# Kernel tuning notes

Measured on AMD Instinct MI355X. Metric: run time of the kernel, lower is better.

The kernel has to match this reference:

```python
import jax, jax.numpy as jnp
import numpy as np

HEAD = 8

def setup_inputs() -> dict:
    key = jax.random.key(0)
    ks = jax.random.split(key, 11)
    B, C, W, H = 16, 512, 32, 32
    d, N = C // HEAD, W * H
    return {
        "x": jax.random.normal(ks[0], (B, C, W, H), jnp.float32),
        "Wq": jax.random.normal(ks[1], (C, C), jnp.float32) * 0.02,
        "bq": jax.random.normal(ks[2], (C,), jnp.float32) * 0.02,
        "Wk": jax.random.normal(ks[3], (C, C), jnp.float32) * 0.02,
        "bk": jax.random.normal(ks[4], (C,), jnp.float32) * 0.02,
        "Wv": jax.random.normal(ks[5], (C, C), jnp.float32) * 0.02,
        "bv": jax.random.normal(ks[6], (C,), jnp.float32) * 0.02,
        "rel_h": jax.random.normal(ks[7], (1, HEAD, d, 1, H), jnp.float32),
        "rel_w": jax.random.normal(ks[8], (1, HEAD, d, W, 1), jnp.float32),
        "reg_qk": jax.random.normal(ks[9], (1, N, N), jnp.float32),
        "reg_v": jax.random.normal(ks[10], (1, d, N), jnp.float32),
    }

def reference(x, Wq, bq, Wk, bk, Wv, bv, rel_h, rel_w, reg_qk, reg_v):
    B, C, W, H = x.shape
    head = HEAD
    d = C // head
    N = W * H
    def conv1x1(inp, Wt, b):  # 1x1 conv == per-pixel linear
        return jnp.einsum('bchw,oc->bohw', inp, Wt) + b[None, :, None, None]
    q = conv1x1(x, Wq, bq).reshape(B, head, d, N)
    k = conv1x1(x, Wk, bk).reshape(B, head, d, N)
    v = conv1x1(x, Wv, bv).reshape(B, head, d, N)
    # content-content: q^T k -> [B, head, N, N]
    cc = jnp.einsum('bhdn,bhdm->bhnm', q, k)
    # content-position: (rel_h + rel_w) broadcast to [1, head, d, W, H] -> [head, N, d]
    pos = (rel_h + rel_w).reshape(head, d, N)
    cp = jnp.einsum('hdn,bhdm->bhnm', pos, q)
    energy = cc + cp  # [B, head, N, N]
    n_reg = reg_qk.shape[0]
    energy = jnp.concatenate(
        [energy, jnp.broadcast_to(reg_qk[None], (B, n_reg, N, N))], axis=1)
    v_all = jnp.concatenate(
        [v, jnp.broadcast_to(reg_v[None], (B, n_reg, d, N))], axis=1)
    attn = jax.nn.softmax(energy, axis=-1)  # [B, head+n_reg, N, N]
    # v @ attn^T
    out = jnp.einsum('bgdn,bgmn->bgdm', v_all, attn)
    out = out[:, :head].reshape(B, C, W, H)
    return out + x
```

## Files before the change

### kernel.cpp

```cpp
#include <hip/hip_runtime.h>

#define BB   16
#define HEADS 8
#define DH   64
#define NSP  1024
#define CCH  512

typedef unsigned int   u32;
typedef unsigned short u16;
typedef __attribute__((ext_vector_type(8))) short  short8;
typedef __attribute__((ext_vector_type(4))) float  floatx4;
typedef __attribute__((ext_vector_type(2))) unsigned uint2v;

#if defined(__has_builtin)
#if __has_builtin(__builtin_amdgcn_exp2f)
#define EXP2F(x) __builtin_amdgcn_exp2f(x)
#else
#define EXP2F(x) exp2f(x)
#endif
#if __has_builtin(__builtin_amdgcn_permlane32_swap)
#define HAVE_PL32 1
#endif
#if __has_builtin(__builtin_amdgcn_permlane16_swap)
#define HAVE_PL16 1
#endif
#else
#define EXP2F(x) exp2f(x)
#endif

__device__ __forceinline__ u16 f2b(float f) {
  u32 x = __float_as_uint(f);
  x = x + 0x7fffu + ((x >> 16) & 1u);
  return (u16)(x >> 16);
}

__device__ __forceinline__ u32 pkbf(float lo, float hi) {
  return __builtin_amdgcn_perm(__float_as_uint(hi) + 0x8000u,
                               __float_as_uint(lo) + 0x8000u, 0x07060302u);
}

__device__ __forceinline__ void gload_lds16(const u16* g, u16* l) {
  __builtin_amdgcn_global_load_lds((const __attribute__((address_space(1))) u32*)g,
                                   (__attribute__((address_space(3))) u32*)l, 16, 0, 0);
}

__device__ __forceinline__ void lane32_swap(u32 a, u32 b, u32& ap, u32& bp, bool hi32) {
#ifdef HAVE_PL32
  uint2v r = __builtin_amdgcn_permlane32_swap(a, b, false, false);
  ap = r.x; bp = r.y;
  (void)hi32;
#else
  u32 sb = (u32)__shfl_xor((int)b, 32);
  u32 sa = (u32)__shfl_xor((int)a, 32);
  ap = hi32 ? sb : a;
  bp = hi32 ? b : sa;
#endif
}

__device__ __forceinline__ u32 lane16_xor(u32 x, bool qodd) {
#ifdef HAVE_PL16
  uint2v r = __builtin_amdgcn_permlane16_swap(x, x, false, false);
  return qodd ? r.x : r.y;
#else
  return (u32)__shfl_xor((int)x, 16);
#endif
}

__global__ __launch_bounds__(256) void prep_all(const float* __restrict__ x,
                                                const float* __restrict__ Wq,
                                                const float* __restrict__ Wk,
                                                const float* __restrict__ Wv,
                                                const float* __restrict__ rel_h,
                                                const float* __restrict__ rel_w,
                                                u16* __restrict__ wbf,
                                                u16* __restrict__ pos,
                                                u16* __restrict__ xt) {
  __shared__ float ld[64][68];
  int bid = blockIdx.x;
  int t = threadIdx.x;
  if (bid < 768) {
    int idx = bid * 256 + t;
    int which = idx >> 16;
    int r4 = (idx & 65535) * 4;
    const float* src = which == 0 ? Wq : which == 1 ? Wk : Wv;
    float4 v = *(const float4*)&src[r4];
    ushort4 s;
    s.x = f2b(v.x); s.y = f2b(v.y); s.z = f2b(v.z); s.w = f2b(v.w);
    *(ushort4*)&wbf[(which << 18) + r4] = s;
  } else if (bid < 2816) {
    int idx = (bid - 768) * 256 + t;
    int dd = idx & 63;
    int n  = (idx >> 6) & 1023;
    int h  = idx >> 16;
    int ww = n >> 5, hh = n & 31;
    float v = rel_h[(h * 64 + dd) * 32 + hh] + rel_w[(h * 64 + dd) * 32 + ww];
    pos[idx] = f2b(v);
  } else {
    int bid2 = bid - 2816;
    int ntile = bid2 & 15, ctile = (bid2 >> 4) & 7, b = bid2 >> 7;
    const float* xb = x + (((size_t)b * CCH + ctile * 64) << 10) + ntile * 64;
#pragma unroll
    for (int p = 0; p < 4; ++p) {
      int c = p * 16 + (t >> 4), n4 = (t & 15) * 4;
      float4 v = *(const float4*)&xb[((size_t)c << 10) + n4];
      ld[c][n4 + 0] = v.x; ld[c][n4 + 1] = v.y; ld[c][n4 + 2] = v.z; ld[c][n4 + 3] = v.w;
    }
    __syncthreads();
    u16* xo = xt + (((size_t)b << 10) + ntile * 64) * CCH + ctile * 64;
#pragma unroll
    for (int p = 0; p < 2; ++p) {
      int id = p * 256 + t;
      int n = id >> 3, c8 = (id & 7) * 8;
      ushort4 s0, s1;
      s0.x = f2b(ld[c8 + 0][n]); s0.y = f2b(ld[c8 + 1][n]);
      s0.z = f2b(ld[c8 + 2][n]); s0.w = f2b(ld[c8 + 3][n]);
      s1.x = f2b(ld[c8 + 4][n]); s1.y = f2b(ld[c8 + 5][n]);
      s1.z = f2b(ld[c8 + 6][n]); s1.w = f2b(ld[c8 + 7][n]);
      *(ushort4*)&xo[(size_t)n * CCH + c8] = s0;
      *(ushort4*)&xo[(size_t)n * CCH + c8 + 4] = s1;
    }
  }
}

__global__ __launch_bounds__(256, 2) void qkv_fused(const u16* __restrict__ wbf,
                                                    const u16* __restrict__ xt,
                                                    const float* __restrict__ bq,
                                                    const float* __restrict__ bk,
                                                    const float* __restrict__ bv,
                                                    u16* __restrict__ qw,
                                                    u16* __restrict__ kw,
                                                    u16* __restrict__ vtw) {
  int hid = blockIdx.x;
  int xcd  = hid & 7;
  int slot = hid >> 3;
  int otile = slot & 7;
  int pair  = xcd * 16 + (slot >> 3);
  int ntile = pair & 7;
  int b     = pair >> 3;
  int o0 = otile * 64, n0 = ntile * 128;

  __shared__ __align__(16) u16 smem[2 * 20480];

  int t = threadIdx.x;
  int w = t >> 6, lane = t & 63;
  int l15 = lane & 15, quad = lane >> 4;
  int srow = lane >> 3, sc = lane & 7;
  int scc = (sc ^ srow) << 3;

  floatx4 aq[8], ak[8], av[8];
#pragma unroll
  for (int i = 0; i < 8; ++i) {
    aq[i] = (floatx4){0.f, 0.f, 0.f, 0.f};
    ak[i] = (floatx4){0.f, 0.f, 0.f, 0.f};
    av[i] = (floatx4){0.f, 0.f, 0.f, 0.f};
  }

  auto stage = [&](int k0, int buf) {
    u16* base = smem + buf * 20480;
#pragma unroll
    for (int p = 0; p < 10; ++p) {
      int g0 = w * 80 + p * 8;
      if (g0 < 192) {
        int which = g0 >> 6;
        int r0 = g0 & 63;
        gload_lds16(wbf + ((size_t)which << 18) + (size_t)(o0 + r0 + srow) * CCH + k0 + scc,
                    base + which * 4096 + r0 * 64);
      } else {
        int r0 = g0 - 192;
        gload_lds16(xt + (size_t)(b * 1024 + n0 + r0 + srow) * CCH + k0 + scc,
                    base + 12288 + r0 * 64);
      }
    }
  };

  int rs = l15 & 7;
  int c0 = (quad ^ rs) << 3;
  int c1 = ((4 + quad) ^ rs) << 3;
  int wrow = (w * 16 + l15) * 64;

  stage(0, 0);
  stage(64, 1);

  for (int ki = 0; ki < 8; ++ki) {
    if (ki < 7) asm volatile("s_waitcnt vmcnt(10)" ::: "memory");
    else        asm volatile("s_waitcnt vmcnt(0)" ::: "memory");
    __builtin_amdgcn_s_barrier();
    __builtin_amdgcn_sched_barrier(0);

    u16* base = smem + (ki & 1) * 20480;
    u16* Xb = base + 12288;
    __builtin_amdgcn_s_setprio(1);
#pragma unroll
    for (int ks = 0; ks < 2; ++ks) {
      int cc = ks ? c1 : c0;
      short8 fq = *(short8*)&base[wrow + cc];
      short8 fk = *(short8*)&base[4096 + wrow + cc];
      short8 fv = *(short8*)&base[8192 + wrow + cc];
#pragma unroll
      for (int ns = 0; ns < 8; ++ns) {
        short8 fx = *(short8*)&Xb[(ns * 16 + l15) * 64 + cc];
        aq[ns] = __builtin_amdgcn_mfma_f32_16x16x32_bf16(fq, fx, aq[ns], 0, 0, 0);
        ak[ns] = __builtin_amdgcn_mfma_f32_16x16x32_bf16(fk, fx, ak[ns], 0, 0, 0);
        av[ns] = __builtin_amdgcn_mfma_f32_16x16x32_bf16(fx, fv, av[ns], 0, 0, 0);
      }
    }
    __builtin_amdgcn_s_setprio(0);

    if (ki < 6) {
      __builtin_amdgcn_sched_barrier(0);
      __builtin_amdgcn_s_barrier();
      stage((ki + 2) * 64, ki & 1);
    }
  }

  __syncthreads();
  u16* epQ = smem;
  u16* epK = smem + 9216;
  u16* epV = smem + 18432;
  {
    int ob = o0 + w * 16 + quad * 4;
    float q0 = bq[ob], q1 = bq[ob + 1], q2 = bq[ob + 2], q3 = bq[ob + 3];
    float k0b = bk[ob], k1b = bk[ob + 1], k2b = bk[ob + 2], k3b = bk[ob + 3];
    float vb = bv[o0 + w * 16 + l15];
#pragma unroll
    for (int ns = 0; ns < 8; ++ns) {
      int n = ns * 16 + l15;
      uint2 pk;
      pk.x = pkbf(aq[ns][0] + q0, aq[ns][1] + q1);
      pk.y = pkbf(aq[ns][2] + q2, aq[ns][3] + q3);
      *(uint2*)&epQ[n * 72 + w * 16 + quad * 4] = pk;
      pk.x = pkbf(ak[ns][0] + k0b, ak[ns][1] + k1b);
      pk.y = pkbf(ak[ns][2] + k2b, ak[ns][3] + k3b);
      *(uint2*)&epK[n * 72 + w * 16 + quad * 4] = pk;
      pk.x = pkbf(av[ns][0] + vb, av[ns][1] + vb);
      pk.y = pkbf(av[ns][2] + vb, av[ns][3] + vb);
      *(uint2*)&epV[(w * 16 + l15) * 136 + ns * 16 + quad * 4] = pk;
    }
  }
  __syncthreads();
  int h = otile;
  {
    int row = t >> 1, half = t & 1;
    size_t gb = ((size_t)(b * HEADS + h) * NSP + n0 + row) * 64 + half * 32;
#pragma unroll
    for (int i = 0; i < 4; ++i)
      *(uint4*)&qw[gb + i * 8] = *(uint4*)&epQ[row * 72 + half * 32 + i * 8];
#pragma unroll
    for (int i = 0; i < 4; ++i)
      *(uint4*)&kw[gb + i * 8] = *(uint4*)&epK[row * 72 + half * 32 + i * 8];
  }
  {
    int row = t >> 2, q4 = t & 3;
#pragma unroll
    for (int i = 0; i < 4; ++i) {
      int nl = q4 * 32 + i * 8;
      int n = n0 + nl;
      int ntl = n >> 6, nn = n & 63;
      *(uint4*)&vtw[(((size_t)(b * HEADS + h) * 16 + ntl) * 64 + row) * 64 + nn]
          = *(uint4*)&epV[row * 136 + nl];
    }
  }
}

__global__ __launch_bounds__(256, 2) void attn_mfma(const u16* __restrict__ qw,
                                                    const u16* __restrict__ kw,
                                                    const u16* __restrict__ vtw,
                                                    const u16* __restrict__ pos,
                                                    const float* __restrict__ x,
                                                    float* __restrict__ out) {
  int bh = blockIdx.x, mtile = blockIdx.y;
  int b = bh >> 3, h = bh & 7;
  __shared__ __align__(16) u16 smem_u16[36864];

  int t = threadIdx.x;
  int w = t >> 6, lane = t & 63;
  int l15 = lane & 15, quad = lane >> 4;
  bool qodd = (quad & 1) != 0;
  bool hi32 = lane >= 32;
  size_t bhs = (size_t)bh;

  short8 qa[4][2], pa[4][2];
  {
    const short* qg = (const short*)qw + (bhs * NSP + mtile * 256 + w * 64) * 64;
    const short* pg = (const short*)pos + ((size_t)h * NSP + mtile * 256 + w * 64) * 64;
#pragma unroll
    for (int msub = 0; msub < 4; ++msub)
#pragma unroll
      for (int ks = 0; ks < 2; ++ks) {
        int off = (msub * 16 + l15) * 64 + ks * 32 + quad * 8;
        qa[msub][ks] = *(const short8*)(qg + off);
        pa[msub][ks] = *(const short8*)(pg + off);
      }
  }

  floatx4 oacc[4][4];
  float lsum[4] = {0.f, 0.f, 0.f, 0.f};
#pragma unroll
  for (int i = 0; i < 4; ++i)
#pragma unroll
    for (int j = 0; j < 4; ++j) oacc[i][j] = (floatx4){0.f, 0.f, 0.f, 0.f};

  const u16* kg  = kw + bhs * NSP * 64;
  const u16* qgn = qw + bhs * NSP * 64;
  const u16* vg  = vtw + bhs * 16 * 4096;
  int srow = lane >> 3, sc = lane & 7;

  int rs = l15 & 7;
  int c0 = (quad ^ rs) << 3;
  int c1 = ((4 + quad) ^ rs) << 3;

  auto stage = [&](int nt, int buf) {
    u16* kt = smem_u16 + buf * 12288;
    u16* qt = kt + 4096;
    u16* vt = qt + 4096;
#pragma unroll
    for (int p = 0; p < 2; ++p) {
      int r0 = w * 16 + p * 8;
      int row = r0 + srow;
      int swz = ((sc ^ (row & 7)) << 3);
      gload_lds16(kg + (nt * 64 + row) * 64 + swz, &kt[r0 * 64]);
      gload_lds16(qgn + (nt * 64 + row) * 64 + swz, &qt[r0 * 64]);
      gload_lds16(vg + (size_t)nt * 4096 + row * 64 + swz, &vt[r0 * 64]);
    }
  };

  stage(0, 0);
  stage(1, 1);

  for (int nt = 0; nt < 16; ++nt) {
    __builtin_amdgcn_s_barrier();
    if (nt < 14) {
      stage(nt + 2, (nt + 2) % 3);
      asm volatile("s_waitcnt vmcnt(12)" ::: "memory");
    } else if (nt == 14) {
      asm volatile("s_waitcnt vmcnt(6)" ::: "memory");
    } else {
      asm volatile("s_waitcnt vmcnt(0)" ::: "memory");
    }
    __builtin_amdgcn_sched_barrier(0);

    u16* kt = smem_u16 + (nt % 3) * 12288;
    u16* qt = kt + 4096;
    u16* vt = qt + 4096;

#pragma unroll
    for (int half = 0; half < 2; ++half) {
      u32 Wd[4][4];
#pragma unroll
      for (int nblk2 = 0; nblk2 < 2; ++nblk2) {
        int nblk = half * 2 + nblk2;
        int rb = (nblk * 16 + l15) * 64;
        short8 kb0 = *(short8*)&kt[rb + c0];
        short8 kb1 = *(short8*)&kt[rb + c1];
        short8 qb0 = *(short8*)&qt[rb + c0];
        short8 qb1 = *(short8*)&qt[rb + c1];
        floatx4 sc4[4];
        __builtin_amdgcn_s_setprio(1);
#pragma unroll
        for (int msub = 0; msub < 4; ++msub) {
          floatx4 c = (floatx4){0.f, 0.f, 0.f, 0.f};
          c = __builtin_amdgcn_mfma_f32_16x16x32_bf16(kb0, qa[msub][0], c, 0, 0, 0);
          c = __builtin_amdgcn_mfma_f32_16x16x32_bf16(kb1, qa[msub][1], c, 0, 0, 0);
          c = __builtin_amdgcn_mfma_f32_16x16x32_bf16(qb0, pa[msub][0], c, 0, 0, 0);
          c = __builtin_amdgcn_mfma_f32_16x16x32_bf16(qb1, pa[msub][1], c, 0, 0, 0);
          sc4[msub] = c;
        }
        __builtin_amdgcn_s_setprio(0);
#pragma unroll
        for (int msub = 0; msub < 4; ++msub) {
          float p0 = EXP2F(fmaf(sc4[msub][0], 1.44269504f, -11.5415603f));
          float p1 = EXP2F(fmaf(sc4[msub][1], 1.44269504f, -11.5415603f));
          float p2 = EXP2F(fmaf(sc4[msub][2], 1.44269504f, -11.5415603f));
          float p3 = EXP2F(fmaf(sc4[msub][3], 1.44269504f, -11.5415603f));
          lsum[msub] += (p0 + p1) + (p2 + p3);
          Wd[msub][nblk2 * 2 + 0] = pkbf(p0, p1);
          Wd[msub][nblk2 * 2 + 1] = pkbf(p2, p3);
        }
      }
      short8 pB[4];
#pragma unroll
      for (int msub = 0; msub < 4; ++msub) {
        u32 A0p, B0p, A1p, B1p;
        lane32_swap(Wd[msub][0], Wd[msub][2], A0p, B0p, hi32);
        lane32_swap(Wd[msub][1], Wd[msub][3], A1p, B1p, hi32);
        u32 G0 = lane16_xor(qodd ? A0p : B0p, qodd);
        u32 G1 = lane16_xor(qodd ? A1p : B1p, qodd);
        union { u32 u[4]; short8 s; } cvt;
        cvt.u[0] = qodd ? G0 : A0p;
        cvt.u[1] = qodd ? G1 : A1p;
        cvt.u[2] = qodd ? B0p : G0;
        cvt.u[3] = qodd ? B1p : G1;
        pB[msub] = cvt.s;
      }
      __builtin_amdgcn_s_setprio(1);
#pragma unroll
      for (int dd = 0; dd < 4; ++dd) {
        int row = dd * 16 + l15;
        short8 vb = *(short8*)&vt[row * 64 + (((half * 4 + quad) ^ (row & 7)) << 3)];
#pragma unroll
        for (int msub = 0; msub < 4; ++msub)
          oacc[msub][dd] = __builtin_amdgcn_mfma_f32_16x16x32_bf16(vb, pB[msub], oacc[msub][dd], 0, 0, 0);
      }
      __builtin_amdgcn_s_setprio(0);
    }
  }

  float rinv[4];
#pragma unroll
  for (int msub = 0; msub < 4; ++msub) {
    float l = lsum[msub];
    l += __shfl_xor(l, 16);
    l += __shfl_xor(l, 32);
    rinv[msub] = 1.0f / l;
  }

  __syncthreads();
  float* ot = (float*)smem_u16 + w * 2304;
  int l8 = lane & 7, lr = lane >> 3;
#pragma unroll
  for (int mh = 0; mh < 2; ++mh) {
#pragma unroll
    for (int ms2 = 0; ms2 < 2; ++ms2) {
      int msub = mh * 2 + ms2;
#pragma unroll
      for (int dd = 0; dd < 4; ++dd)
#pragma unroll
        for (int r = 0; r < 4; ++r)
          ot[(dd * 16 + quad * 4 + r) * 36 + ms2 * 16 + l15] = oacc[msub][dd][r] * rinv[msub];
    }
#pragma unroll
    for (int pass = 0; pass < 8; ++pass) {
      int dd = pass * 8 + lr;
      float4 o4 = *(float4*)&ot[dd * 36 + l8 * 4];
      size_t off = (((size_t)b * CCH + h * DH + dd) << 10) + mtile * 256 + w * 64 + mh * 32 + l8 * 4;
      float4 xv = *(const float4*)&x[off];
      o4.x += xv.x; o4.y += xv.y; o4.z += xv.z; o4.w += xv.w;
      *(float4*)&out[off] = o4;
    }
  }
}

extern "C" void kernel_launch(void* const* d_in, const int* in_sizes, int n_in,
                              void* d_out, int out_size, void* d_ws, size_t ws_size,
                              hipStream_t stream) {
  const float* x     = (const float*)d_in[0];
  const float* Wq    = (const float*)d_in[1];
  const float* bq    = (const float*)d_in[2];
  const float* Wk    = (const float*)d_in[3];
  const float* bk    = (const float*)d_in[4];
  const float* Wv    = (const float*)d_in[5];
  const float* bv    = (const float*)d_in[6];
  const float* rel_h = (const float*)d_in[7];
  const float* rel_w = (const float*)d_in[8];
  float* out = (float*)d_out;

  char* ws = (char*)d_ws;
  u16* qw   = (u16*)(ws);
  u16* kw   = (u16*)(ws + ((size_t)16 << 20));
  u16* vtw  = (u16*)(ws + ((size_t)32 << 20));
  u16* pos  = (u16*)(ws + ((size_t)48 << 20));
  u16* wbf  = (u16*)(ws + ((size_t)49 << 20));
  u16* xt   = (u16*)d_out;

  hipLaunchKernelGGL(prep_all, dim3(4864), dim3(256), 0, stream,
                     x, Wq, Wk, Wv, rel_h, rel_w, wbf, pos, xt);
  hipLaunchKernelGGL(qkv_fused, dim3(1024), dim3(256), 0, stream,
                     wbf, xt, bq, bk, bv, qw, kw, vtw);
  hipLaunchKernelGGL(attn_mfma, dim3(128, 4), dim3(256), 0, stream,
                     qw, kw, vtw, pos, x, out);
}
```

Baseline: 208.0 us.

## Switch attention kernel to 32x32x16 MFMA tiles and drop setprio hints

```diff
diff --git a/kernel.cpp b/kernel.cpp
--- a/kernel.cpp
+++ b/kernel.cpp
@@ -10,6 +10,7 @@
 typedef unsigned short u16;
 typedef __attribute__((ext_vector_type(8))) short  short8;
 typedef __attribute__((ext_vector_type(4))) float  floatx4;
+typedef __attribute__((ext_vector_type(16))) float floatx16;
 typedef __attribute__((ext_vector_type(2))) unsigned uint2v;
 
 #if defined(__has_builtin)
@@ -20,9 +21,6 @@
 #endif
 #if __has_builtin(__builtin_amdgcn_permlane32_swap)
 #define HAVE_PL32 1
-#endif
-#if __has_builtin(__builtin_amdgcn_permlane16_swap)
-#define HAVE_PL16 1
 #endif
 #else
 #define EXP2F(x) exp2f(x)
@@ -54,15 +52,6 @@
   u32 sa = (u32)__shfl_xor((int)a, 32);
   ap = hi32 ? sb : a;
   bp = hi32 ? b : sa;
-#endif
-}
-
-__device__ __forceinline__ u32 lane16_xor(u32 x, bool qodd) {
-#ifdef HAVE_PL16
-  uint2v r = __builtin_amdgcn_permlane16_swap(x, x, false, false);
-  return qodd ? r.x : r.y;
-#else
-  return (u32)__shfl_xor((int)x, 16);
 #endif
 }
 
@@ -189,7 +178,6 @@
 
     u16* base = smem + (ki & 1) * 20480;
     u16* Xb = base + 12288;
-    __builtin_amdgcn_s_setprio(1);
 #pragma unroll
     for (int ks = 0; ks < 2; ++ks) {
       int cc = ks ? c1 : c0;
@@ -204,7 +192,6 @@
         av[ns] = __builtin_amdgcn_mfma_f32_16x16x32_bf16(fx, fv, av[ns], 0, 0, 0);
       }
     }
-    __builtin_amdgcn_s_setprio(0);
 
     if (ki < 6) {
       __builtin_amdgcn_sched_barrier(0);
@@ -274,40 +261,38 @@
 
   int t = threadIdx.x;
   int w = t >> 6, lane = t & 63;
-  int l15 = lane & 15, quad = lane >> 4;
-  bool qodd = (quad & 1) != 0;
-  bool hi32 = lane >= 32;
+  int l31 = lane & 31, hi1 = lane >> 5;
+  int hi8 = hi1 * 8;
+  bool hi32 = hi1 != 0;
   size_t bhs = (size_t)bh;
 
-  short8 qa[4][2], pa[4][2];
+  short8 qa[2][4], pa[2][4];
   {
     const short* qg = (const short*)qw + (bhs * NSP + mtile * 256 + w * 64) * 64;
     const short* pg = (const short*)pos + ((size_t)h * NSP + mtile * 256 + w * 64) * 64;
 #pragma unroll
-    for (int msub = 0; msub < 4; ++msub)
-#pragma unroll
-      for (int ks = 0; ks < 2; ++ks) {
-        int off = (msub * 16 + l15) * 64 + ks * 32 + quad * 8;
+    for (int msub = 0; msub < 2; ++msub)
+#pragma unroll
+      for (int ks = 0; ks < 4; ++ks) {
+        int off = (msub * 32 + l31) * 64 + ks * 16 + hi8;
         qa[msub][ks] = *(const short8*)(qg + off);
         pa[msub][ks] = *(const short8*)(pg + off);
       }
   }
 
-  floatx4 oacc[4][4];
-  float lsum[4] = {0.f, 0.f, 0.f, 0.f};
-#pragma unroll
-  for (int i = 0; i < 4; ++i)
-#pragma unroll
-    for (int j = 0; j < 4; ++j) oacc[i][j] = (floatx4){0.f, 0.f, 0.f, 0.f};
+  floatx16 oacc[2][2];
+  float lsum[2] = {0.f, 0.f};
+#pragma unroll
+  for (int i = 0; i < 2; ++i)
+#pragma unroll
+    for (int j = 0; j < 2; ++j)
+#pragma unroll
+      for (int r = 0; r < 16; ++r) oacc[i][j][r] = 0.f;
 
   const u16* kg  = kw + bhs * NSP * 64;
   const u16* qgn = qw + bhs * NSP * 64;
   const u16* vg  = vtw + bhs * 16 * 4096;
   int srow = lane >> 3, sc = lane & 7;
-
-  int rs = l15 & 7;
-  int c0 = (quad ^ rs) << 3;
-  int c1 = ((4 + quad) ^ rs) << 3;
 
   auto stage = [&](int nt, int buf) {
     u16* kt = smem_u16 + buf * 12288;
@@ -344,72 +329,66 @@
     u16* vt = qt + 4096;
 
 #pragma unroll
-    for (int half = 0; half < 2; ++half) {
-      u32 Wd[4][4];
-#pragma unroll
-      for (int nblk2 = 0; nblk2 < 2; ++nblk2) {
-        int nblk = half * 2 + nblk2;
-        int rb = (nblk * 16 + l15) * 64;
-        short8 kb0 = *(short8*)&kt[rb + c0];
-        short8 kb1 = *(short8*)&kt[rb + c1];
-        short8 qb0 = *(short8*)&qt[rb + c0];
-        short8 qb1 = *(short8*)&qt[rb + c1];
-        floatx4 sc4[4];
-        __builtin_amdgcn_s_setprio(1);
-#pragma unroll
-        for (int msub = 0; msub < 4; ++msub) {
-          floatx4 c = (floatx4){0.f, 0.f, 0.f, 0.f};
-          c = __builtin_amdgcn_mfma_f32_16x16x32_bf16(kb0, qa[msub][0], c, 0, 0, 0);
-          c = __builtin_amdgcn_mfma_f32_16x16x32_bf16(kb1, qa[msub][1], c, 0, 0, 0);
-          c = __builtin_amdgcn_mfma_f32_16x16x32_bf16(qb0, pa[msub][0], c, 0, 0, 0);
-          c = __builtin_amdgcn_mfma_f32_16x16x32_bf16(qb1, pa[msub][1], c, 0, 0, 0);
-          sc4[msub] = c;
+    for (int nsub = 0; nsub < 2; ++nsub) {
+      short8 kf[4], qf[4];
+      int rowA = nsub * 32 + l31, rx7 = rowA & 7;
+#pragma unroll
+      for (int ks = 0; ks < 4; ++ks) {
+        int ad = rowA * 64 + (((ks * 2 + hi1) ^ rx7) << 3);
+        kf[ks] = *(short8*)&kt[ad];
+        qf[ks] = *(short8*)&qt[ad];
+      }
+      short8 pv0[2], pv1[2];
+#pragma unroll
+      for (int msub = 0; msub < 2; ++msub) {
+        floatx16 c;
+#pragma unroll
+        for (int r = 0; r < 16; ++r) c[r] = 0.f;
+#pragma unroll
+        for (int ks = 0; ks < 4; ++ks)
+          c = __builtin_amdgcn_mfma_f32_32x32x16_bf16(kf[ks], qa[msub][ks], c, 0, 0, 0);
+#pragma unroll
+        for (int ks = 0; ks < 4; ++ks)
+          c = __builtin_amdgcn_mfma_f32_32x32x16_bf16(qf[ks], pa[msub][ks], c, 0, 0, 0);
+        float p[16];
+#pragma unroll
+        for (int r = 0; r < 16; ++r)
+          p[r] = EXP2F(fmaf(c[r], 1.44269504f, -11.5415603f));
+        lsum[msub] += (((p[0] + p[1]) + (p[2] + p[3])) + ((p[4] + p[5]) + (p[6] + p[7])))
+                    + (((p[8] + p[9]) + (p[10] + p[11])) + ((p[12] + p[13]) + (p[14] + p[15])));
+        u32 wp[8];
+#pragma unroll
+        for (int i = 0; i < 8; ++i) wp[i] = pkbf(p[2 * i], p[2 * i + 1]);
+        u32 x0, y0, x1, y1, x2, y2, x3, y3;
+        lane32_swap(wp[0], wp[2], x0, y0, hi32);
+        lane32_swap(wp[1], wp[3], x1, y1, hi32);
+        lane32_swap(wp[4], wp[6], x2, y2, hi32);
+        lane32_swap(wp[5], wp[7], x3, y3, hi32);
+        union { u32 u[4]; short8 s; } cv0, cv1;
+        cv0.u[0] = x0; cv0.u[1] = x1; cv0.u[2] = y0; cv0.u[3] = y1;
+        cv1.u[0] = x2; cv1.u[1] = x3; cv1.u[2] = y2; cv1.u[3] = y3;
+        pv0[msub] = cv0.s;
+        pv1[msub] = cv1.s;
+      }
+#pragma unroll
+      for (int ddsub = 0; ddsub < 2; ++ddsub) {
+        int rowV = ddsub * 32 + l31, rv7 = rowV & 7;
+        int ksb = nsub * 2;
+        short8 v0 = *(short8*)&vt[rowV * 64 + ((((ksb + 0) * 2 + hi1) ^ rv7) << 3)];
+        short8 v1 = *(short8*)&vt[rowV * 64 + ((((ksb + 1) * 2 + hi1) ^ rv7) << 3)];
+#pragma unroll
+        for (int msub = 0; msub < 2; ++msub) {
+          oacc[msub][ddsub] = __builtin_amdgcn_mfma_f32_32x32x16_bf16(v0, pv0[msub], oacc[msub][ddsub], 0, 0, 0);
+          oacc[msub][ddsub] = __builtin_amdgcn_mfma_f32_32x32x16_bf16(v1, pv1[msub], oacc[msub][ddsub], 0, 0, 0);
         }
-        __builtin_amdgcn_s_setprio(0);
-#pragma unroll
-        for (int msub = 0; msub < 4; ++msub) {
-          float p0 = EXP2F(fmaf(sc4[msub][0], 1.44269504f, -11.5415603f));
-          float p1 = EXP2F(fmaf(sc4[msub][1], 1.44269504f, -11.5415603f));
-          float p2 = EXP2F(fmaf(sc4[msub][2], 1.44269504f, -11.5415603f));
-          float p3 = EXP2F(fmaf(sc4[msub][3], 1.44269504f, -11.5415603f));
-          lsum[msub] += (p0 + p1) + (p2 + p3);
-          Wd[msub][nblk2 * 2 + 0] = pkbf(p0, p1);
-          Wd[msub][nblk2 * 2 + 1] = pkbf(p2, p3);
-        }
-      }
-      short8 pB[4];
-#pragma unroll
-      for (int msub = 0; msub < 4; ++msub) {
-        u32 A0p, B0p, A1p, B1p;
-        lane32_swap(Wd[msub][0], Wd[msub][2], A0p, B0p, hi32);
-        lane32_swap(Wd[msub][1], Wd[msub][3], A1p, B1p, hi32);
-        u32 G0 = lane16_xor(qodd ? A0p : B0p, qodd);
-        u32 G1 = lane16_xor(qodd ? A1p : B1p, qodd);
-        union { u32 u[4]; short8 s; } cvt;
-        cvt.u[0] = qodd ? G0 : A0p;
-        cvt.u[1] = qodd ? G1 : A1p;
-        cvt.u[2] = qodd ? B0p : G0;
-        cvt.u[3] = qodd ? B1p : G1;
-        pB[msub] = cvt.s;
-      }
-      __builtin_amdgcn_s_setprio(1);
-#pragma unroll
-      for (int dd = 0; dd < 4; ++dd) {
-        int row = dd * 16 + l15;
-        short8 vb = *(short8*)&vt[row * 64 + (((half * 4 + quad) ^ (row & 7)) << 3)];
-#pragma unroll
-        for (int msub = 0; msub < 4; ++msub)
-          oacc[msub][dd] = __builtin_amdgcn_mfma_f32_16x16x32_bf16(vb, pB[msub], oacc[msub][dd], 0, 0, 0);
-      }
-      __builtin_amdgcn_s_setprio(0);
-    }
-  }
-
-  float rinv[4];
-#pragma unroll
-  for (int msub = 0; msub < 4; ++msub) {
+      }
+    }
+  }
+
+  float rinv[2];
+#pragma unroll
+  for (int msub = 0; msub < 2; ++msub) {
     float l = lsum[msub];
-    l += __shfl_xor(l, 16);
     l += __shfl_xor(l, 32);
     rinv[msub] = 1.0f / l;
   }
@@ -420,14 +399,12 @@
 #pragma unroll
   for (int mh = 0; mh < 2; ++mh) {
 #pragma unroll
-    for (int ms2 = 0; ms2 < 2; ++ms2) {
-      int msub = mh * 2 + ms2;
-#pragma unroll
-      for (int dd = 0; dd < 4; ++dd)
-#pragma unroll
-        for (int r = 0; r < 4; ++r)
-          ot[(dd * 16 + quad * 4 + r) * 36 + ms2 * 16 + l15] = oacc[msub][dd][r] * rinv[msub];
-    }
+    for (int ddsub = 0; ddsub < 2; ++ddsub)
+#pragma unroll
+      for (int r = 0; r < 16; ++r) {
+        int dd = ddsub * 32 + (r & 3) + 8 * (r >> 2) + 4 * hi1;
+        ot[dd * 36 + l31] = oacc[mh][ddsub][r] * rinv[mh];
+      }
 #pragma unroll
     for (int pass = 0; pass < 8; ++pass) {
       int dd = pass * 8 + lr;
```

Result: slower. 216.8 us (+4.2%).

## Pre-swizzle Q/K/V/pos into MFMA fragment layout and load directly to registers

Applied to the files above, without the earlier changes.

```diff
diff --git a/kernel.cpp b/kernel.cpp
--- a/kernel.cpp
+++ b/kernel.cpp
@@ -65,6 +65,7 @@
   return (u32)__shfl_xor((int)x, 16);
 #endif
 }
+
 
 __global__ __launch_bounds__(256) void prep_all(const float* __restrict__ x,
                                                 const float* __restrict__ Wq,
@@ -91,10 +92,13 @@
     int idx = (bid - 768) * 256 + t;
     int dd = idx & 63;
     int n  = (idx >> 6) & 1023;
-    int h  = idx >> 16;
+    int hd = idx >> 16;
     int ww = n >> 5, hh = n & 31;
-    float v = rel_h[(h * 64 + dd) * 32 + hh] + rel_w[(h * 64 + dd) * 32 + ww];
-    pos[idx] = f2b(v);
+    float v = rel_h[(hd * 64 + dd) * 32 + hh] + rel_w[(hd * 64 + dd) * 32 + ww];
+    int ntp = n >> 6, nbp = (n >> 4) & 3, rp = n & 15;
+    int ksp = dd >> 5, qp = (dd >> 3) & 3, ep = dd & 7;
+    size_t off = ((((size_t)(hd * 16 + ntp) * 4 + nbp) * 2 + ksp) * 64 + qp * 16 + rp) * 8 + ep;
+    pos[off] = f2b(v);
   } else {
     int bid2 = bid - 2816;
     int ntile = bid2 & 15, ctile = (bid2 >> 4) & 7, b = bid2 >> 7;
@@ -189,7 +193,6 @@
 
     u16* base = smem + (ki & 1) * 20480;
     u16* Xb = base + 12288;
-    __builtin_amdgcn_s_setprio(1);
 #pragma unroll
     for (int ks = 0; ks < 2; ++ks) {
       int cc = ks ? c1 : c0;
@@ -204,7 +207,6 @@
         av[ns] = __builtin_amdgcn_mfma_f32_16x16x32_bf16(fx, fv, av[ns], 0, 0, 0);
       }
     }
-    __builtin_amdgcn_s_setprio(0);
 
     if (ki < 6) {
       __builtin_amdgcn_sched_barrier(0);
@@ -239,25 +241,31 @@
   }
   __syncthreads();
   int h = otile;
+  size_t bhI = (size_t)(b * HEADS + h);
   {
     int row = t >> 1, half = t & 1;
-    size_t gb = ((size_t)(b * HEADS + h) * NSP + n0 + row) * 64 + half * 32;
+    int nt_ = (n0 + row) >> 6;
+    int nblk_ = (row >> 4) & 3;
+    int r_ = row & 15;
+    size_t qkbase = (((bhI * 16 + nt_) * 4 + nblk_) * 2 + half) * 512;
 #pragma unroll
     for (int i = 0; i < 4; ++i)
-      *(uint4*)&qw[gb + i * 8] = *(uint4*)&epQ[row * 72 + half * 32 + i * 8];
+      *(uint4*)&qw[qkbase + (i * 16 + r_) * 8] = *(uint4*)&epQ[row * 72 + half * 32 + i * 8];
 #pragma unroll
     for (int i = 0; i < 4; ++i)
-      *(uint4*)&kw[gb + i * 8] = *(uint4*)&epK[row * 72 + half * 32 + i * 8];
+      *(uint4*)&kw[qkbase + (i * 16 + r_) * 8] = *(uint4*)&epK[row * 72 + half * 32 + i * 8];
   }
   {
     int row = t >> 2, q4 = t & 3;
+    int ddblk = row >> 4, r_ = row & 15;
 #pragma unroll
     for (int i = 0; i < 4; ++i) {
       int nl = q4 * 32 + i * 8;
       int n = n0 + nl;
-      int ntl = n >> 6, nn = n & 63;
-      *(uint4*)&vtw[(((size_t)(b * HEADS + h) * 16 + ntl) * 64 + row) * 64 + nn]
-          = *(uint4*)&epV[row * 136 + nl];
+      int ntv = n >> 6, np = n & 63;
+      int nh = np >> 5, q = (np >> 3) & 3;
+      size_t vbase = (((bhI * 16 + ntv) * 4 + ddblk) * 2 + nh) * 512;
+      *(uint4*)&vtw[vbase + (q * 16 + r_) * 8] = *(uint4*)&epV[row * 136 + nl];
     }
   }
 }
@@ -270,7 +278,7 @@
                                                     float* __restrict__ out) {
   int bh = blockIdx.x, mtile = blockIdx.y;
   int b = bh >> 3, h = bh & 7;
-  __shared__ __align__(16) u16 smem_u16[36864];
+  __shared__ __align__(16) float smem_f[9216];
 
   int t = threadIdx.x;
   int w = t >> 6, lane = t & 63;
@@ -278,18 +286,19 @@
   bool qodd = (quad & 1) != 0;
   bool hi32 = lane >= 32;
   size_t bhs = (size_t)bh;
+  int lane8 = lane * 8;
 
   short8 qa[4][2], pa[4][2];
   {
-    const short* qg = (const short*)qw + (bhs * NSP + mtile * 256 + w * 64) * 64;
-    const short* pg = (const short*)pos + ((size_t)h * NSP + mtile * 256 + w * 64) * 64;
+    const u16* qmb = qw + bhs * 65536 + (size_t)(mtile * 4 + w) * 4096;
+    const u16* pmb = pos + (size_t)h * 65536 + (size_t)(mtile * 4 + w) * 4096;
 #pragma unroll
     for (int msub = 0; msub < 4; ++msub)
 #pragma unroll
       for (int ks = 0; ks < 2; ++ks) {
-        int off = (msub * 16 + l15) * 64 + ks * 32 + quad * 8;
-        qa[msub][ks] = *(const short8*)(qg + off);
-        pa[msub][ks] = *(const short8*)(pg + off);
+        int off = (msub * 2 + ks) * 512 + lane8;
+        qa[msub][ks] = *(const short8*)(qmb + off);
+        pa[msub][ks] = *(const short8*)(pmb + off);
       }
   }
 
@@ -300,48 +309,29 @@
 #pragma unroll
     for (int j = 0; j < 4; ++j) oacc[i][j] = (floatx4){0.f, 0.f, 0.f, 0.f};
 
-  const u16* kg  = kw + bhs * NSP * 64;
-  const u16* qgn = qw + bhs * NSP * 64;
-  const u16* vg  = vtw + bhs * 16 * 4096;
-  int srow = lane >> 3, sc = lane & 7;
-
-  int rs = l15 & 7;
-  int c0 = (quad ^ rs) << 3;
-  int c1 = ((4 + quad) ^ rs) << 3;
-
-  auto stage = [&](int nt, int buf) {
-    u16* kt = smem_u16 + buf * 12288;
-    u16* qt = kt + 4096;
-    u16* vt = qt + 4096;
-#pragma unroll
-    for (int p = 0; p < 2; ++p) {
-      int r0 = w * 16 + p * 8;
-      int row = r0 + srow;
-      int swz = ((sc ^ (row & 7)) << 3);
-      gload_lds16(kg + (nt * 64 + row) * 64 + swz, &kt[r0 * 64]);
-      gload_lds16(qgn + (nt * 64 + row) * 64 + swz, &qt[r0 * 64]);
-      gload_lds16(vg + (size_t)nt * 4096 + row * 64 + swz, &vt[r0 * 64]);
-    }
-  };
-
-  stage(0, 0);
-  stage(1, 1);
+  const u16* kg = kw + bhs * 65536;
+  const u16* qg = qw + bhs * 65536;
+  const u16* vg = vtw + bhs * 65536;
 
   for (int nt = 0; nt < 16; ++nt) {
-    __builtin_amdgcn_s_barrier();
-    if (nt < 14) {
-      stage(nt + 2, (nt + 2) % 3);
-      asm volatile("s_waitcnt vmcnt(12)" ::: "memory");
-    } else if (nt == 14) {
-      asm volatile("s_waitcnt vmcnt(6)" ::: "memory");
-    } else {
-      asm volatile("s_waitcnt vmcnt(0)" ::: "memory");
-    }
-    __builtin_amdgcn_sched_barrier(0);
-
-    u16* kt = smem_u16 + (nt % 3) * 12288;
-    u16* qt = kt + 4096;
-    u16* vt = qt + 4096;
+    const u16* kgt = kg + nt * 4096;
+    const u16* qgt = qg + nt * 4096;
+    const u16* vgt = vg + nt * 4096;
+
+    short8 kb[4][2], qb[4][2], vb[4][2];
+#pragma unroll
+    for (int nblk = 0; nblk < 4; ++nblk)
+#pragma unroll
+      for (int ks = 0; ks < 2; ++ks) {
+        int off = (nblk * 2 + ks) * 512 + lane8;
+        kb[nblk][ks] = *(const short8*)(kgt + off);
+        qb[nblk][ks] = *(const short8*)(qgt + off);
+      }
+#pragma unroll
+    for (int dd = 0; dd < 4; ++dd)
+#pragma unroll
+      for (int hf = 0; hf < 2; ++hf)
+        vb[dd][hf] = *(const short8*)(vgt + (dd * 2 + hf) * 512 + lane8);
 
 #pragma unroll
     for (int half = 0; half < 2; ++half) {
@@ -349,23 +339,16 @@
 #pragma unroll
       for (int nblk2 = 0; nblk2 < 2; ++nblk2) {
         int nblk = half * 2 + nblk2;
-        int rb = (nblk * 16 + l15) * 64;
-        short8 kb0 = *(short8*)&kt[rb + c0];
-        short8 kb1 = *(short8*)&kt[rb + c1];
-        short8 qb0 = *(short8*)&qt[rb + c0];
-        short8 qb1 = *(short8*)&qt[rb + c1];
         floatx4 sc4[4];
-        __builtin_amdgcn_s_setprio(1);
 #pragma unroll
         for (int msub = 0; msub < 4; ++msub) {
           floatx4 c = (floatx4){0.f, 0.f, 0.f, 0.f};
-          c = __builtin_amdgcn_mfma_f32_16x16x32_bf16(kb0, qa[msub][0], c, 0, 0, 0);
-          c = __builtin_amdgcn_mfma_f32_16x16x32_bf16(kb1, qa[msub][1], c, 0, 0, 0);
-          c = __builtin_amdgcn_mfma_f32_16x16x32_bf16(qb0, pa[msub][0], c, 0, 0, 0);
-          c = __builtin_amdgcn_mfma_f32_16x16x32_bf16(qb1, pa[msub][1], c, 0, 0, 0);
+          c = __builtin_amdgcn_mfma_f32_16x16x32_bf16(kb[nblk][0], qa[msub][0], c, 0, 0, 0);
+          c = __builtin_amdgcn_mfma_f32_16x16x32_bf16(kb[nblk][1], qa[msub][1], c, 0, 0, 0);
+          c = __builtin_amdgcn_mfma_f32_16x16x32_bf16(qb[nblk][0], pa[msub][0], c, 0, 0, 0);
+          c = __builtin_amdgcn_mfma_f32_16x16x32_bf16(qb[nblk][1], pa[msub][1], c, 0, 0, 0);
           sc4[msub] = c;
         }
-        __builtin_amdgcn_s_setprio(0);
 #pragma unroll
         for (int msub = 0; msub < 4; ++msub) {
           float p0 = EXP2F(fmaf(sc4[msub][0], 1.44269504f, -11.5415603f));
@@ -392,16 +375,12 @@
         cvt.u[3] = qodd ? B1p : G1;
         pB[msub] = cvt.s;
       }
-      __builtin_amdgcn_s_setprio(1);
 #pragma unroll
       for (int dd = 0; dd < 4; ++dd) {
-        int row = dd * 16 + l15;
-        short8 vb = *(short8*)&vt[row * 64 + (((half * 4 + quad) ^ (row & 7)) << 3)];
 #pragma unroll
         for (int msub = 0; msub < 4; ++msub)
-          oacc[msub][dd] = __builtin_amdgcn_mfma_f32_16x16x32_bf16(vb, pB[msub], oacc[msub][dd], 0, 0, 0);
-      }
-      __builtin_amdgcn_s_setprio(0);
+          oacc[msub][dd] = __builtin_amdgcn_mfma_f32_16x16x32_bf16(vb[dd][half], pB[msub], oacc[msub][dd], 0, 0, 0);
+      }
     }
   }
 
@@ -414,8 +393,7 @@
     rinv[msub] = 1.0f / l;
   }
 
-  __syncthreads();
-  float* ot = (float*)smem_u16 + w * 2304;
+  float* ot = smem_f + w * 2304;
   int l8 = lane & 7, lr = lane >> 3;
 #pragma unroll
   for (int mh = 0; mh < 2; ++mh) {
```

New measurement: 199.3 us. -4.2%, faster.
